# Optimization experiments

Hardware: AMD Instinct MI355X
Metric: run time of the kernel (lower is better)

Reference implementation:

```python
import jax, jax.numpy as jnp
import numpy as np

B, S, D, H = 2, 2048, 1024, 16
DH = D // H

def setup_inputs() -> dict:
    key = jax.random.key(0)
    ks = jax.random.split(key, 12)
    def lin(kw, kb, fan_in):
        bound = 1.0 / np.sqrt(fan_in)
        W = jax.random.uniform(kw, (D, D), jnp.float32, -bound, bound)
        b = jax.random.uniform(kb, (D,), jnp.float32, -bound, bound)
        return W, b
    Wq, bq = lin(ks[0], ks[1], D)
    Wk, bk = lin(ks[2], ks[3], D)
    Wv, bv = lin(ks[4], ks[5], D)
    Wo, bo = lin(ks[6], ks[7], D)
    q = jax.random.normal(ks[8], (B, S, D), jnp.float32)
    k = jax.random.normal(ks[9], (B, S, D), jnp.float32)
    v = jax.random.normal(ks[10], (B, S, D), jnp.float32)
    # causal mask (1 = keep, 0 = masked), broadcastable to [B,H,S,S]
    mask = jnp.tril(jnp.ones((S, S), jnp.int32))[None, None, :, :]
    return {"q": q, "k": k, "v": v, "mask": mask,
            "Wq": Wq, "bq": bq, "Wk": Wk, "bk": bk,
            "Wv": Wv, "bv": bv, "Wo": Wo, "bo": bo}

def reference(q, k, v, mask, Wq, bq, Wk, bk, Wv, bv, Wo, bo):
    # projections: torch Linear is x @ W.T + b
    def split(x):  # [B,S,D] -> [B,H,S,DH]
        return x.reshape(B, S, H, DH).transpose(0, 2, 1, 3)
    qh = split(q @ Wq.T + bq)
    kh = split(k @ Wk.T + bk)
    vh = split(v @ Wv.T + bv)
    score = jnp.einsum('bhqd,bhkd->bhqk', qh, kh) / jnp.sqrt(jnp.float32(DH))
    score = jnp.where(mask == 0, jnp.float32(-1e9), score)
    attn = jax.nn.softmax(score, axis=-1)
    out = jnp.einsum('bhqk,bhkd->bhqd', attn, vh)
    out = out.transpose(0, 2, 1, 3).reshape(B, S, D)
    return out @ Wo.T + bo, attn
```

## Files before the change

kernel.cpp:

```cpp
#include <hip/hip_runtime.h>

#define S_LEN 2048
#define D_MODEL 1024
#define N_HEADS 16
#define D_HEAD 64
#define BATCH 2

typedef __bf16 bf16;
typedef __bf16 bf16x8 __attribute__((ext_vector_type(8)));
typedef __bf16 bf16x4 __attribute__((ext_vector_type(4)));
typedef float f32x4 __attribute__((ext_vector_type(4)));

__device__ __forceinline__ f32x4 mfma16(bf16x8 a, bf16x8 b, f32x4 c) {
  return __builtin_amdgcn_mfma_f32_16x16x32_bf16(a, b, c, 0, 0, 0);
}

__device__ __forceinline__ void gload16(const bf16* g, bf16* lds) {
  __builtin_amdgcn_global_load_lds((const __attribute__((address_space(1))) void*)g,
                                   (__attribute__((address_space(3))) void*)lds, 16, 0, 0);
}

__global__ __launch_bounds__(256) void cvt_w(
    const float* __restrict__ s0, const float* __restrict__ s1,
    const float* __restrict__ s2, const float* __restrict__ s3,
    bf16* __restrict__ d0, bf16* __restrict__ d1, bf16* __restrict__ d2,
    bf16* __restrict__ d3) {
  const int y = blockIdx.y;
  const float* s = (y == 0) ? s0 : (y == 1) ? s1 : (y == 2) ? s2 : s3;
  bf16* d = (y == 0) ? d0 : (y == 1) ? d1 : (y == 2) ? d2 : d3;
  const int i = blockIdx.x * blockDim.x + threadIdx.x;
  const f32x4 a = *(const f32x4*)(s + (size_t)i * 8);
  const f32x4 b = *(const f32x4*)(s + (size_t)i * 8 + 4);
  bf16x8 o;
  o[0] = (bf16)a[0]; o[1] = (bf16)a[1]; o[2] = (bf16)a[2]; o[3] = (bf16)a[3];
  o[4] = (bf16)b[0]; o[5] = (bf16)b[1]; o[6] = (bf16)b[2]; o[7] = (bf16)b[3];
  *(bf16x8*)(d + (size_t)i * 8) = o;
}

__device__ __forceinline__ void gemm_loop(const bf16* __restrict__ gA,
                                          const bf16* __restrict__ gB,
                                          bf16* As, bf16* Bs,
                                          f32x4 (&acc)[4][4], int tid) {
  const int l = tid & 63;
  const int w = tid >> 6;
  const int wr = w >> 1, wc = w & 1;
  const int lr = l & 15, lg = l >> 4;
  const int rl = l >> 2;
  const int c8l = l & 3;
  const int chA = lg ^ ((lr >> 1) & 3);

#define STAGE_PAIR(ks, buf)                                                   \
  {                                                                           \
    _Pragma("unroll") for (int i = 0; i < 2; ++i) {                           \
      const int blk = w + i * 4;                                              \
      const int row = blk * 16 + rl;                                          \
      const int s8 = c8l ^ ((row >> 1) & 3);                                  \
      gload16(gA + (size_t)row * D_MODEL + (ks) * 32 + s8 * 8,                \
              As + (buf) * 4096 + blk * 512);                                 \
      gload16(gB + (size_t)row * D_MODEL + (ks) * 32 + s8 * 8,                \
              Bs + (buf) * 4096 + blk * 512);                                 \
    }                                                                         \
  }

  STAGE_PAIR(0, 0);
  __syncthreads();
  int cur = 0;
  for (int ks = 0; ks < 32; ++ks) {
    if (ks < 31) STAGE_PAIR(ks + 1, cur ^ 1);
    bf16x8 af[4], bfb[4];
#pragma unroll
    for (int mm = 0; mm < 4; ++mm)
      af[mm] = *(const bf16x8*)(As + cur * 4096 + (wr * 64 + mm * 16 + lr) * 32 + chA * 8);
#pragma unroll
    for (int nn = 0; nn < 4; ++nn)
      bfb[nn] = *(const bf16x8*)(Bs + cur * 4096 + (wc * 64 + nn * 16 + lr) * 32 + chA * 8);
#pragma unroll
    for (int mm = 0; mm < 4; ++mm)
#pragma unroll
      for (int nn = 0; nn < 4; ++nn)
        acc[mm][nn] = mfma16(af[mm], bfb[nn], acc[mm][nn]);
    __syncthreads();
    cur ^= 1;
  }
#undef STAGE_PAIR
}

__device__ __forceinline__ void gemm_loop_af32(const float* __restrict__ gA32,
                                               const bf16* __restrict__ gB,
                                               bf16* As, bf16* Bs,
                                               f32x4 (&acc)[4][4], int tid) {
  const int l = tid & 63;
  const int w = tid >> 6;
  const int wr = w >> 1, wc = w & 1;
  const int lr = l & 15, lg = l >> 4;
  const int rl = l >> 2, c8l = l & 3;
  const int chA = lg ^ ((lr >> 1) & 3);

  const int arow = tid >> 1;
  const int ahalf = tid & 1;
  const float* aptr = gA32 + (size_t)arow * D_MODEL + ahalf * 16;
  const int asw = (arow >> 1) & 3;

#define LOAD_A(ks, av)                                                        \
  _Pragma("unroll") for (int c = 0; c < 4; ++c)                               \
      av[c] = *(const f32x4*)(aptr + (ks) * 32 + c * 4);

#define WRITE_A(buf, av)                                                      \
  {                                                                           \
    _Pragma("unroll") for (int j = 0; j < 2; ++j) {                           \
      bf16x8 o;                                                               \
      _Pragma("unroll") for (int e = 0; e < 4; ++e) {                         \
        o[e] = (bf16)av[j * 2][e];                                            \
        o[e + 4] = (bf16)av[j * 2 + 1][e];                                    \
      }                                                                       \
      const int c8 = ahalf * 2 + j;                                           \
      *(bf16x8*)(As + (buf) * 4096 + arow * 32 + (c8 ^ asw) * 8) = o;         \
    }                                                                         \
  }

#define STAGE_B(ks, buf)                                                      \
  {                                                                           \
    _Pragma("unroll") for (int i = 0; i < 2; ++i) {                           \
      const int blk = w + i * 4;                                              \
      const int row = blk * 16 + rl;                                          \
      const int s8 = c8l ^ ((row >> 1) & 3);                                  \
      gload16(gB + (size_t)row * D_MODEL + (ks) * 32 + s8 * 8,                \
              Bs + (buf) * 4096 + blk * 512);                                 \
    }                                                                         \
  }

  {
    f32x4 av[4];
    LOAD_A(0, av);
    STAGE_B(0, 0);
    WRITE_A(0, av);
  }
  __syncthreads();
  int cur = 0;
  for (int ks = 0; ks < 32; ++ks) {
    f32x4 av[4];
    if (ks < 31) {
      LOAD_A(ks + 1, av);
      STAGE_B(ks + 1, cur ^ 1);
    }
    bf16x8 af[4], bfb[4];
#pragma unroll
    for (int mm = 0; mm < 4; ++mm)
      af[mm] = *(const bf16x8*)(As + cur * 4096 + (wr * 64 + mm * 16 + lr) * 32 + chA * 8);
#pragma unroll
    for (int nn = 0; nn < 4; ++nn)
      bfb[nn] = *(const bf16x8*)(Bs + cur * 4096 + (wc * 64 + nn * 16 + lr) * 32 + chA * 8);
#pragma unroll
    for (int mm = 0; mm < 4; ++mm)
#pragma unroll
      for (int nn = 0; nn < 4; ++nn)
        acc[mm][nn] = mfma16(af[mm], bfb[nn], acc[mm][nn]);
    if (ks < 31) WRITE_A(cur ^ 1, av);
    __syncthreads();
    cur ^= 1;
  }
#undef LOAD_A
#undef WRITE_A
#undef STAGE_B
}

__global__ __launch_bounds__(256) void gemm_qkv(
    const float* __restrict__ qf, const float* __restrict__ kf,
    const float* __restrict__ vf, const bf16* __restrict__ Wqb,
    const bf16* __restrict__ Wkb, const bf16* __restrict__ Wvb,
    const float* __restrict__ biasq, const float* __restrict__ biask,
    const float* __restrict__ biasv, bf16* __restrict__ qhw,
    bf16* __restrict__ khw, bf16* __restrict__ vtw) {
  __shared__ __align__(16) char smem[32768];
  bf16* As = (bf16*)smem;
  bf16* Bs = (bf16*)(smem + 16384);
  typedef bf16 Trow[72];
  Trow* T = (Trow*)smem;
  const int z = blockIdx.z;
  const float* A = (z == 0) ? qf : (z == 1) ? kf : vf;
  const bf16* W = (z == 0) ? Wqb : (z == 1) ? Wkb : Wvb;
  const float* bias = (z == 0) ? biasq : (z == 1) ? biask : biasv;
  const float scale = (z == 0) ? 0.125f : 1.0f;
  bf16* out = (z == 0) ? qhw : (z == 1) ? khw : vtw;

  const int tid = threadIdx.x;
  const int l = tid & 63;
  const int w = tid >> 6;
  const int wr = w >> 1, wc = w & 1;
  const int lr = l & 15, lg = l >> 4;

  f32x4 acc[4][4] = {};
  gemm_loop_af32(A + ((size_t)blockIdx.x * 128) * D_MODEL,
                 W + ((size_t)blockIdx.y * 128) * D_MODEL, As, Bs, acc, tid);

  const int b = (blockIdx.x * 128) >> 11;
  const int s0 = (blockIdx.x * 128) & 2047;

  if (z == 2) {
#pragma unroll
    for (int half = 0; half < 2; ++half) {
      if (wc == half) {
#pragma unroll
        for (int nn = 0; nn < 4; ++nn) {
          const int n = blockIdx.y * 128 + half * 64 + nn * 16 + lr;
          const float bv = bias[n];
#pragma unroll
          for (int mm = 0; mm < 4; ++mm)
#pragma unroll
            for (int r = 0; r < 4; ++r) {
              const int ml = wr * 64 + mm * 16 + lg * 4 + r;
              T[ml][nn * 16 + lr] = (bf16)(acc[mm][nn][r] + bv);
            }
        }
      }
      __syncthreads();
      const int d = tid & 63;
      const int sblk = (tid >> 6) * 32;
      const int hglob = blockIdx.y * 2 + half;
      bf16* orow = vtw + (((size_t)(b * N_HEADS + hglob)) * D_HEAD + d) * S_LEN + s0 + sblk;
#pragma unroll
      for (int j = 0; j < 4; ++j) {
        bf16x8 pk;
#pragma unroll
        for (int e = 0; e < 8; ++e) pk[e] = T[sblk + j * 8 + e][d];
        *(bf16x8*)(orow + j * 8) = pk;
      }
      __syncthreads();
    }
  } else {
#pragma unroll
    for (int half = 0; half < 2; ++half) {
      if (wc == half) {
#pragma unroll
        for (int nn = 0; nn < 4; ++nn) {
          const int n = blockIdx.y * 128 + half * 64 + nn * 16 + lr;
          const float bv = bias[n];
#pragma unroll
          for (int mm = 0; mm < 4; ++mm)
#pragma unroll
            for (int r = 0; r < 4; ++r) {
              const int ml = wr * 64 + mm * 16 + lg * 4 + r;
              T[ml][nn * 16 + lr] = (bf16)((acc[mm][nn][r] + bv) * scale);
            }
        }
      }
      __syncthreads();
      const int hglob = blockIdx.y * 2 + half;
      bf16* obase = out + ((size_t)(b * N_HEADS + hglob) * S_LEN + s0) * D_HEAD;
      const int rsub = tid >> 3;
      const int d8 = (tid & 7) * 8;
#pragma unroll
      for (int j = 0; j < 4; ++j) {
        const int row_l = j * 32 + rsub;
        *(bf16x8*)(obase + (size_t)row_l * D_HEAD + d8) = *(const bf16x8*)(&T[row_l][d8]);
      }
      __syncthreads();
    }
  }
}

__device__ __forceinline__ void stage_strip(const bf16* __restrict__ src,
                                            size_t rstride, bf16* lds, int tid) {
#pragma unroll
  for (int rnd = 0; rnd < 2; ++rnd) {
    const int chunk = rnd * 256 + tid;
    const int row = chunk >> 3;
    const int c8 = chunk & 7;
    const int src8 = c8 ^ (row & 7);
    gload16(src + (size_t)row * rstride + src8 * 8, lds + chunk * 8);
  }
}

__global__ __launch_bounds__(256) void attn_flash(
    const bf16* __restrict__ qh, const bf16* __restrict__ kh,
    const bf16* __restrict__ vt, bf16* __restrict__ ctx,
    float* __restrict__ lbuf, float* __restrict__ attn) {
  __shared__ bf16 Kb[2][64 * 64];
  __shared__ bf16 Vb[2][64 * 64];
  __shared__ bf16 P[4][16][72];
  const int tid = threadIdx.x;
  const int w = tid >> 6, l = tid & 63;
  const int lr = l & 15, lg = l >> 4;
  const int bh = blockIdx.y;
  const int bxx = blockIdx.x;

  if (bxx >= 32) {
    int rem = bxx - 32, zq = 0, cnt = 7;
    while (rem >= cnt) { rem -= cnt; --cnt; ++zq; }
    const int kq = zq + 1 + rem;
    float* base = attn + (size_t)bh * S_LEN * S_LEN + (size_t)(zq * 256) * S_LEN + kq * 256;
    const f32x4 zv = {};
    for (int it = 0; it < 64; ++it) {
      float* rp = base + (size_t)(it * 4 + w) * S_LEN + l * 4;
      __builtin_nontemporal_store(zv, (f32x4*)rp);
    }
    return;
  }

  const int qgroup = (bxx & 1) ? (31 - (bxx >> 1)) : (bxx >> 1);
  const int q0 = qgroup * 64 + w * 16;
  const int qrow = q0 + lr;
  const bf16* qp = qh + (size_t)bh * S_LEN * D_HEAD;
  const bf16* kp = kh + (size_t)bh * S_LEN * D_HEAD;
  const bf16* vp = vt + (size_t)bh * D_HEAD * S_LEN;

  const bf16x8 qf0 = *(const bf16x8*)(qp + (size_t)qrow * D_HEAD + lg * 8);
  const bf16x8 qf1 = *(const bf16x8*)(qp + (size_t)qrow * D_HEAD + 32 + lg * 8);

  const float NINF = -__builtin_inff();
  const int nfull = qgroup;
  const int x0 = (lg ^ (lr & 7)) * 8;
  const int x1 = ((4 | lg) ^ (lr & 7)) * 8;

  stage_strip(kp, D_HEAD, Kb[0], tid);
  stage_strip(vp, S_LEN, Vb[0], tid);
  __syncthreads();

  float lsum = 0.f;
  f32x4 oacc[4] = {};
  int cur = 0;

  for (int st = 0; st < nfull; ++st) {
    stage_strip(kp + (size_t)(st + 1) * 64 * D_HEAD, D_HEAD, Kb[cur ^ 1], tid);
    stage_strip(vp + (st + 1) * 64, S_LEN, Vb[cur ^ 1], tid);

    float ps = 0.f;
    __builtin_amdgcn_s_setprio(1);
    f32x4 zz4[4];
#pragma unroll
    for (int t = 0; t < 4; ++t) {
      const bf16* krow = Kb[cur] + (t * 16 + lr) * 64;
      f32x4 zz = {};
      zz = mfma16(*(const bf16x8*)(krow + x0), qf0, zz);
      zz = mfma16(*(const bf16x8*)(krow + x1), qf1, zz);
      zz4[t] = zz;
    }
    __builtin_amdgcn_s_setprio(0);
#pragma unroll
    for (int t = 0; t < 4; ++t) {
      bf16x4 pk;
#pragma unroll
      for (int r = 0; r < 4; ++r) {
        const float e = __expf(fminf(zz4[t][r], 60.f));
        ps += e;
        pk[r] = (bf16)e;
      }
      *(bf16x4*)(&P[w][lr][t * 16 + lg * 4]) = pk;
    }
    ps += __shfl_xor(ps, 16);
    ps += __shfl_xor(ps, 32);
    lsum += ps;
    const bf16x8 pb0 = *(const bf16x8*)(&P[w][lr][lg * 8]);
    const bf16x8 pb1 = *(const bf16x8*)(&P[w][lr][32 + lg * 8]);
    __builtin_amdgcn_s_setprio(1);
#pragma unroll
    for (int dt = 0; dt < 4; ++dt) {
      const bf16* vrow = Vb[cur] + (dt * 16 + lr) * 64;
      oacc[dt] = mfma16(*(const bf16x8*)(vrow + x0), pb0, oacc[dt]);
      oacc[dt] = mfma16(*(const bf16x8*)(vrow + x1), pb1, oacc[dt]);
    }
    __builtin_amdgcn_s_setprio(0);
    __syncthreads();
    cur ^= 1;
  }

  {
    float ps = 0.f;
#pragma unroll
    for (int t = 0; t < 4; ++t) {
      bf16x4 pk;
      if (t <= w) {
        const bf16* krow = Kb[cur] + (t * 16 + lr) * 64;
        f32x4 zz = {};
        zz = mfma16(*(const bf16x8*)(krow + x0), qf0, zz);
        zz = mfma16(*(const bf16x8*)(krow + x1), qf1, zz);
#pragma unroll
        for (int r = 0; r < 4; ++r) {
          const float sv = (t == w && (lg * 4 + r) > lr) ? NINF : zz[r];
          const float e = __expf(fminf(sv, 60.f));
          ps += e;
          pk[r] = (bf16)e;
        }
      } else {
#pragma unroll
        for (int r = 0; r < 4; ++r) pk[r] = (bf16)0.f;
      }
      *(bf16x4*)(&P[w][lr][t * 16 + lg * 4]) = pk;
    }
    ps += __shfl_xor(ps, 16);
    ps += __shfl_xor(ps, 32);
    lsum += ps;
    const bf16x8 pb0 = *(const bf16x8*)(&P[w][lr][lg * 8]);
    const bf16x8 pb1 = *(const bf16x8*)(&P[w][lr][32 + lg * 8]);
#pragma unroll
    for (int dt = 0; dt < 4; ++dt) {
      const bf16* vrow = Vb[cur] + (dt * 16 + lr) * 64;
      oacc[dt] = mfma16(*(const bf16x8*)(vrow + x0), pb0, oacc[dt]);
      oacc[dt] = mfma16(*(const bf16x8*)(vrow + x1), pb1, oacc[dt]);
    }
  }

  const float invl = 1.0f / lsum;
  const int b = bh >> 4, h = bh & 15;
  bf16* crow = ctx + ((size_t)(b * S_LEN + qrow)) * D_MODEL + h * D_HEAD;
#pragma unroll
  for (int dt = 0; dt < 4; ++dt) {
    bf16x4 ov;
#pragma unroll
    for (int r = 0; r < 4; ++r) ov[r] = (bf16)(oacc[dt][r] * invl);
    *(bf16x4*)(crow + dt * 16 + lg * 4) = ov;
  }
  if (lg == 0) lbuf[(size_t)bh * S_LEN + qrow] = invl;
}

__global__ __launch_bounds__(256) void mat_out(
    const bf16* __restrict__ qh, const bf16* __restrict__ kh,
    const float* __restrict__ lbuf, float* __restrict__ attn,
    const bf16* __restrict__ ctxA, const bf16* __restrict__ Wo,
    const float* __restrict__ bo, float* __restrict__ outp) {
  __shared__ __align__(16) char smem[34048];
  const int bid = blockIdx.x;
  const int tid = threadIdx.x;
  const int w = tid >> 6, l = tid & 63;
  const int lr = l & 15, lg = l >> 4;

  if (bid < 256) {
    bf16* As = (bf16*)smem;
    bf16* Bs = (bf16*)(smem + 16384);
    const int bx = bid & 31, by = bid >> 5;
    const int wr = w >> 1, wc = w & 1;
    f32x4 acc[4][4] = {};
    gemm_loop(ctxA + ((size_t)bx * 128) * D_MODEL,
              Wo + ((size_t)by * 128) * D_MODEL, As, Bs, acc, tid);
    const int rowg0 = bx * 128 + wr * 64;
    const int colg0 = by * 128 + wc * 64;
#pragma unroll
    for (int nn = 0; nn < 4; ++nn) {
      const int n = colg0 + nn * 16 + lr;
      const float bv = bo[n];
#pragma unroll
      for (int mm = 0; mm < 4; ++mm)
#pragma unroll
        for (int r = 0; r < 4; ++r) {
          const int m = rowg0 + mm * 16 + lg * 4 + r;
          __builtin_nontemporal_store(acc[mm][nn][r] + bv,
                                      outp + (size_t)m * D_MODEL + n);
        }
    }
    return;
  }

  bf16* Pt = (bf16*)smem;
  const int mid = bid - 256;
  const int bh = mid / 144;
  int rem = mid - bh * 144;
  int g = 0;
  while (2 * (g + 1) * (g + 2) <= rem) ++g;
  const int rem2 = rem - 2 * g * (g + 1);
  const int q0t = 4 * g + rem2 / (g + 1);
  const int kq = rem2 - (g + 1) * (rem2 / (g + 1));
  const int q0 = q0t * 64;
  const int k0b = kq * 256;
  float* ap = attn + (size_t)bh * S_LEN * S_LEN;

  const int k0 = k0b + w * 64;
  if (k0 <= q0 + 63) {
    const bf16* qp = qh + (size_t)bh * S_LEN * D_HEAD;
    const bf16* kp = kh + (size_t)bh * S_LEN * D_HEAD;
    float iv[4];
#pragma unroll
    for (int qs = 0; qs < 4; ++qs)
      iv[qs] = lbuf[(size_t)bh * S_LEN + q0 + qs * 16 + lr];
    bf16x8 kf[4][2], qf[4][2];
#pragma unroll
    for (int kt = 0; kt < 4; ++kt) {
      kf[kt][0] = *(const bf16x8*)(kp + (size_t)(k0 + kt * 16 + lr) * D_HEAD + lg * 8);
      kf[kt][1] = *(const bf16x8*)(kp + (size_t)(k0 + kt * 16 + lr) * D_HEAD + 32 + lg * 8);
    }
#pragma unroll
    for (int qs = 0; qs < 4; ++qs) {
      qf[qs][0] = *(const bf16x8*)(qp + (size_t)(q0 + qs * 16 + lr) * D_HEAD + lg * 8);
      qf[qs][1] = *(const bf16x8*)(qp + (size_t)(q0 + qs * 16 + lr) * D_HEAD + 32 + lg * 8);
    }
    f32x4 acc[4][4] = {};
#pragma unroll
    for (int qs = 0; qs < 4; ++qs)
#pragma unroll
      for (int kt = 0; kt < 4; ++kt) {
        acc[qs][kt] = mfma16(kf[kt][0], qf[qs][0], acc[qs][kt]);
        acc[qs][kt] = mfma16(kf[kt][1], qf[qs][1], acc[qs][kt]);
      }
#pragma unroll
    for (int qs = 0; qs < 4; ++qs) {
      const int q = q0 + qs * 16 + lr;
#pragma unroll
      for (int kt = 0; kt < 4; ++kt) {
        const int kbase = k0 + kt * 16 + lg * 4;
        bf16x4 pk;
#pragma unroll
        for (int r = 0; r < 4; ++r) {
          const float pv = (kbase + r > q)
                               ? 0.f
                               : __expf(fminf(acc[qs][kt][r], 60.f)) * iv[qs];
          pk[r] = (bf16)pv;
        }
        *(bf16x4*)(Pt + (qs * 16 + lr) * 264 + w * 64 + kt * 16 + lg * 4) = pk;
      }
    }
  } else {
    const bf16x4 z4 = {};
#pragma unroll
    for (int j = 0; j < 16; ++j)
      *(bf16x4*)(Pt + (j * 4 + lg) * 264 + w * 64 + lr * 4) = z4;
  }
  __syncthreads();

#pragma unroll
  for (int j = 0; j < 16; ++j) {
    const int rowl = w * 16 + j;
    const bf16x4 pk = *(const bf16x4*)(Pt + rowl * 264 + l * 4);
    f32x4 o;
    o[0] = (float)pk[0]; o[1] = (float)pk[1];
    o[2] = (float)pk[2]; o[3] = (float)pk[3];
    __builtin_nontemporal_store(
        o, (f32x4*)(ap + (size_t)(q0 + rowl) * S_LEN + k0b + l * 4));
  }
}

extern "C" void kernel_launch(void* const* d_in, const int* in_sizes, int n_in,
                              void* d_out, int out_size, void* d_ws, size_t ws_size,
                              hipStream_t stream) {
  (void)in_sizes; (void)n_in; (void)out_size; (void)ws_size;
  const float* q  = (const float*)d_in[0];
  const float* k  = (const float*)d_in[1];
  const float* v  = (const float*)d_in[2];
  const float* Wq = (const float*)d_in[4];
  const float* bq = (const float*)d_in[5];
  const float* Wk = (const float*)d_in[6];
  const float* bk = (const float*)d_in[7];
  const float* Wv = (const float*)d_in[8];
  const float* bv = (const float*)d_in[9];
  const float* Wo = (const float*)d_in[10];
  const float* bo = (const float*)d_in[11];

  float* outp = (float*)d_out;
  float* attn = outp + (size_t)BATCH * S_LEN * D_MODEL;

  char* ws = (char*)d_ws;
  bf16* qhw  = (bf16*)(ws);
  bf16* khw  = (bf16*)(ws + (8u << 20));
  bf16* vtw  = (bf16*)(ws + (16u << 20));
  bf16* ctxb = (bf16*)(ws + (24u << 20));
  bf16* Wqb  = (bf16*)(ws + (32u << 20));
  bf16* Wkb  = (bf16*)(ws + (34u << 20));
  bf16* Wvb  = (bf16*)(ws + (36u << 20));
  bf16* Wob  = (bf16*)(ws + (38u << 20));
  float* lbuf = (float*)(ws + (40u << 20));

  dim3 bb(256);
  cvt_w<<<dim3(512, 4), bb, 0, stream>>>(Wq, Wk, Wv, Wo, Wqb, Wkb, Wvb, Wob);
  gemm_qkv<<<dim3(32, 8, 3), bb, 0, stream>>>(q, k, v, Wqb, Wkb, Wvb,
                                              bq, bk, bv, qhw, khw, vtw);
  attn_flash<<<dim3(60, 32), bb, 0, stream>>>(qhw, khw, vtw, ctxb, lbuf, attn);
  mat_out<<<dim3(256 + 4608), bb, 0, stream>>>(qhw, khw, lbuf, attn,
                                               ctxb, Wob, bo, outp);
}
```

Measured before the change: 236.6 us.

## Fuse attention-probability writeback into flash kernel via second K pass

The flash attention kernel now does a second pass over K after computing the row normalizer. It recomputes QK^T, normalizes the scores and writes the probability matrix (plus zeros for the masked tail) directly, instead of leaving that to a separate kernel that read lbuf. This removes the lbuf buffer and the extra launch that mixed the output GEMM with attention-map tiles, and the output GEMM becomes a standalone launch. The cost is that flash blocks now recompute QK and carry the large fp32 attention store serially, which could lengthen the critical path and worsen load imbalance across blocks.

Measured after the change: 241.3 us. No clear change (+2.0%).

```diff
diff --git a/kernel.cpp b/kernel.cpp
--- a/kernel.cpp
+++ b/kernel.cpp
@@ -271,10 +271,10 @@
   }
 }
 
-__global__ __launch_bounds__(256) void attn_flash(
+__global__ __launch_bounds__(256) void attn_fused(
     const bf16* __restrict__ qh, const bf16* __restrict__ kh,
     const bf16* __restrict__ vt, bf16* __restrict__ ctx,
-    float* __restrict__ lbuf, float* __restrict__ attn) {
+    float* __restrict__ attn) {
   __shared__ bf16 Kb[2][64 * 64];
   __shared__ bf16 Vb[2][64 * 64];
   __shared__ bf16 P[4][16][72];
@@ -303,12 +303,14 @@
   const bf16* qp = qh + (size_t)bh * S_LEN * D_HEAD;
   const bf16* kp = kh + (size_t)bh * S_LEN * D_HEAD;
   const bf16* vp = vt + (size_t)bh * D_HEAD * S_LEN;
+  float* ap = attn + (size_t)bh * S_LEN * S_LEN;
 
   const bf16x8 qf0 = *(const bf16x8*)(qp + (size_t)qrow * D_HEAD + lg * 8);
   const bf16x8 qf1 = *(const bf16x8*)(qp + (size_t)qrow * D_HEAD + 32 + lg * 8);
 
   const float NINF = -__builtin_inff();
   const int nfull = qgroup;
+  const int ktail = ((qgroup >> 2) << 2) + 4;
   const int x0 = (lg ^ (lr & 7)) * 8;
   const int x1 = ((4 | lg) ^ (lr & 7)) * 8;
 
@@ -410,120 +412,121 @@
     for (int r = 0; r < 4; ++r) ov[r] = (bf16)(oacc[dt][r] * invl);
     *(bf16x4*)(crow + dt * 16 + lg * 4) = ov;
   }
-  if (lg == 0) lbuf[(size_t)bh * S_LEN + qrow] = invl;
-}
-
-__global__ __launch_bounds__(256) void mat_out(
-    const bf16* __restrict__ qh, const bf16* __restrict__ kh,
-    const float* __restrict__ lbuf, float* __restrict__ attn,
-    const bf16* __restrict__ ctxA, const bf16* __restrict__ Wo,
-    const float* __restrict__ bo, float* __restrict__ outp) {
-  __shared__ __align__(16) char smem[34048];
-  const int bid = blockIdx.x;
+
+  stage_strip(kp, D_HEAD, Kb[cur ^ 1], tid);
+  __syncthreads();
+  cur ^= 1;
+
+  for (int st = 0; st < nfull; ++st) {
+    stage_strip(kp + (size_t)(st + 1) * 64 * D_HEAD, D_HEAD, Kb[cur ^ 1], tid);
+    __builtin_amdgcn_s_setprio(1);
+    f32x4 zz4[4];
+#pragma unroll
+    for (int t = 0; t < 4; ++t) {
+      const bf16* krow = Kb[cur] + (t * 16 + lr) * 64;
+      f32x4 zz = {};
+      zz = mfma16(*(const bf16x8*)(krow + x0), qf0, zz);
+      zz = mfma16(*(const bf16x8*)(krow + x1), qf1, zz);
+      zz4[t] = zz;
+    }
+    __builtin_amdgcn_s_setprio(0);
+#pragma unroll
+    for (int t = 0; t < 4; ++t) {
+      bf16x4 pk;
+#pragma unroll
+      for (int r = 0; r < 4; ++r)
+        pk[r] = (bf16)(__expf(fminf(zz4[t][r], 60.f)) * invl);
+      *(bf16x4*)(&P[w][lr][t * 16 + lg * 4]) = pk;
+    }
+#pragma unroll
+    for (int j = 0; j < 4; ++j) {
+      const int row = j * 4 + lg;
+      const bf16x4 pk4 = *(const bf16x4*)(&P[w][row][lr * 4]);
+      f32x4 o;
+      o[0] = (float)pk4[0]; o[1] = (float)pk4[1];
+      o[2] = (float)pk4[2]; o[3] = (float)pk4[3];
+      __builtin_nontemporal_store(
+          o, (f32x4*)(ap + (size_t)(q0 + row) * S_LEN + st * 64 + lr * 4));
+    }
+    __syncthreads();
+    cur ^= 1;
+  }
+
+  {
+    const int st = nfull;
+#pragma unroll
+    for (int t = 0; t < 4; ++t) {
+      bf16x4 pk;
+      if (t <= w) {
+        const bf16* krow = Kb[cur] + (t * 16 + lr) * 64;
+        f32x4 zz = {};
+        zz = mfma16(*(const bf16x8*)(krow + x0), qf0, zz);
+        zz = mfma16(*(const bf16x8*)(krow + x1), qf1, zz);
+#pragma unroll
+        for (int r = 0; r < 4; ++r) {
+          const float sv = (t == w && (lg * 4 + r) > lr) ? NINF : zz[r];
+          pk[r] = (bf16)(__expf(fminf(sv, 60.f)) * invl);
+        }
+      } else {
+#pragma unroll
+        for (int r = 0; r < 4; ++r) pk[r] = (bf16)0.f;
+      }
+      *(bf16x4*)(&P[w][lr][t * 16 + lg * 4]) = pk;
+    }
+#pragma unroll
+    for (int j = 0; j < 4; ++j) {
+      const int row = j * 4 + lg;
+      const bf16x4 pk4 = *(const bf16x4*)(&P[w][row][lr * 4]);
+      f32x4 o;
+      o[0] = (float)pk4[0]; o[1] = (float)pk4[1];
+      o[2] = (float)pk4[2]; o[3] = (float)pk4[3];
+      __builtin_nontemporal_store(
+          o, (f32x4*)(ap + (size_t)(q0 + row) * S_LEN + st * 64 + lr * 4));
+    }
+  }
+
+  for (int st = nfull + 1; st < ktail; ++st) {
+    const f32x4 zv = {};
+#pragma unroll
+    for (int j = 0; j < 4; ++j) {
+      const int row = j * 4 + lg;
+      __builtin_nontemporal_store(
+          zv, (f32x4*)(ap + (size_t)(q0 + row) * S_LEN + st * 64 + lr * 4));
+    }
+  }
+}
+
+__global__ __launch_bounds__(256) void gemm_out(const bf16* __restrict__ A,
+                                                const bf16* __restrict__ W,
+                                                const float* __restrict__ bias,
+                                                float* __restrict__ out) {
+  __shared__ __align__(16) char smem[32768];
+  bf16* As = (bf16*)smem;
+  bf16* Bs = (bf16*)(smem + 16384);
   const int tid = threadIdx.x;
-  const int w = tid >> 6, l = tid & 63;
+  const int l = tid & 63;
+  const int w = tid >> 6;
+  const int wr = w >> 1, wc = w & 1;
   const int lr = l & 15, lg = l >> 4;
 
-  if (bid < 256) {
-    bf16* As = (bf16*)smem;
-    bf16* Bs = (bf16*)(smem + 16384);
-    const int bx = bid & 31, by = bid >> 5;
-    const int wr = w >> 1, wc = w & 1;
-    f32x4 acc[4][4] = {};
-    gemm_loop(ctxA + ((size_t)bx * 128) * D_MODEL,
-              Wo + ((size_t)by * 128) * D_MODEL, As, Bs, acc, tid);
-    const int rowg0 = bx * 128 + wr * 64;
-    const int colg0 = by * 128 + wc * 64;
-#pragma unroll
-    for (int nn = 0; nn < 4; ++nn) {
-      const int n = colg0 + nn * 16 + lr;
-      const float bv = bo[n];
-#pragma unroll
-      for (int mm = 0; mm < 4; ++mm)
-#pragma unroll
-        for (int r = 0; r < 4; ++r) {
-          const int m = rowg0 + mm * 16 + lg * 4 + r;
-          __builtin_nontemporal_store(acc[mm][nn][r] + bv,
-                                      outp + (size_t)m * D_MODEL + n);
-        }
-    }
-    return;
-  }
-
-  bf16* Pt = (bf16*)smem;
-  const int mid = bid - 256;
-  const int bh = mid / 144;
-  int rem = mid - bh * 144;
-  int g = 0;
-  while (2 * (g + 1) * (g + 2) <= rem) ++g;
-  const int rem2 = rem - 2 * g * (g + 1);
-  const int q0t = 4 * g + rem2 / (g + 1);
-  const int kq = rem2 - (g + 1) * (rem2 / (g + 1));
-  const int q0 = q0t * 64;
-  const int k0b = kq * 256;
-  float* ap = attn + (size_t)bh * S_LEN * S_LEN;
-
-  const int k0 = k0b + w * 64;
-  if (k0 <= q0 + 63) {
-    const bf16* qp = qh + (size_t)bh * S_LEN * D_HEAD;
-    const bf16* kp = kh + (size_t)bh * S_LEN * D_HEAD;
-    float iv[4];
-#pragma unroll
-    for (int qs = 0; qs < 4; ++qs)
-      iv[qs] = lbuf[(size_t)bh * S_LEN + q0 + qs * 16 + lr];
-    bf16x8 kf[4][2], qf[4][2];
-#pragma unroll
-    for (int kt = 0; kt < 4; ++kt) {
-      kf[kt][0] = *(const bf16x8*)(kp + (size_t)(k0 + kt * 16 + lr) * D_HEAD + lg * 8);
-      kf[kt][1] = *(const bf16x8*)(kp + (size_t)(k0 + kt * 16 + lr) * D_HEAD + 32 + lg * 8);
-    }
-#pragma unroll
-    for (int qs = 0; qs < 4; ++qs) {
-      qf[qs][0] = *(const bf16x8*)(qp + (size_t)(q0 + qs * 16 + lr) * D_HEAD + lg * 8);
-      qf[qs][1] = *(const bf16x8*)(qp + (size_t)(q0 + qs * 16 + lr) * D_HEAD + 32 + lg * 8);
-    }
-    f32x4 acc[4][4] = {};
-#pragma unroll
-    for (int qs = 0; qs < 4; ++qs)
-#pragma unroll
-      for (int kt = 0; kt < 4; ++kt) {
-        acc[qs][kt] = mfma16(kf[kt][0], qf[qs][0], acc[qs][kt]);
-        acc[qs][kt] = mfma16(kf[kt][1], qf[qs][1], acc[qs][kt]);
-      }
-#pragma unroll
-    for (int qs = 0; qs < 4; ++qs) {
-      const int q = q0 + qs * 16 + lr;
-#pragma unroll
-      for (int kt = 0; kt < 4; ++kt) {
-        const int kbase = k0 + kt * 16 + lg * 4;
-        bf16x4 pk;
-#pragma unroll
-        for (int r = 0; r < 4; ++r) {
-          const float pv = (kbase + r > q)
-                               ? 0.f
-                               : __expf(fminf(acc[qs][kt][r], 60.f)) * iv[qs];
-          pk[r] = (bf16)pv;
-        }
-        *(bf16x4*)(Pt + (qs * 16 + lr) * 264 + w * 64 + kt * 16 + lg * 4) = pk;
-      }
-    }
-  } else {
-    const bf16x4 z4 = {};
-#pragma unroll
-    for (int j = 0; j < 16; ++j)
-      *(bf16x4*)(Pt + (j * 4 + lg) * 264 + w * 64 + lr * 4) = z4;
-  }
-  __syncthreads();
-
-#pragma unroll
-  for (int j = 0; j < 16; ++j) {
-    const int rowl = w * 16 + j;
-    const bf16x4 pk = *(const bf16x4*)(Pt + rowl * 264 + l * 4);
-    f32x4 o;
-    o[0] = (float)pk[0]; o[1] = (float)pk[1];
-    o[2] = (float)pk[2]; o[3] = (float)pk[3];
-    __builtin_nontemporal_store(
-        o, (f32x4*)(ap + (size_t)(q0 + rowl) * S_LEN + k0b + l * 4));
+  f32x4 acc[4][4] = {};
+  gemm_loop(A + ((size_t)blockIdx.x * 128) * D_MODEL,
+            W + ((size_t)blockIdx.y * 128) * D_MODEL, As, Bs, acc, tid);
+
+  const int rowg0 = blockIdx.x * 128 + wr * 64;
+  const int colg0 = blockIdx.y * 128 + wc * 64;
+#pragma unroll
+  for (int nn = 0; nn < 4; ++nn) {
+    const int n = colg0 + nn * 16 + lr;
+    const float bv = bias[n];
+#pragma unroll
+    for (int mm = 0; mm < 4; ++mm)
+#pragma unroll
+      for (int r = 0; r < 4; ++r) {
+        const int m = rowg0 + mm * 16 + lg * 4 + r;
+        __builtin_nontemporal_store(acc[mm][nn][r] + bv,
+                                    out + (size_t)m * D_MODEL + n);
+      }
   }
 }
 
@@ -555,13 +558,11 @@
   bf16* Wkb  = (bf16*)(ws + (34u << 20));
   bf16* Wvb  = (bf16*)(ws + (36u << 20));
   bf16* Wob  = (bf16*)(ws + (38u << 20));
-  float* lbuf = (float*)(ws + (40u << 20));
 
   dim3 bb(256);
   cvt_w<<<dim3(512, 4), bb, 0, stream>>>(Wq, Wk, Wv, Wo, Wqb, Wkb, Wvb, Wob);
   gemm_qkv<<<dim3(32, 8, 3), bb, 0, stream>>>(q, k, v, Wqb, Wkb, Wvb,
                                               bq, bk, bv, qhw, khw, vtw);
-  attn_flash<<<dim3(60, 32), bb, 0, stream>>>(qhw, khw, vtw, ctxb, lbuf, attn);
-  mat_out<<<dim3(256 + 4608), bb, 0, stream>>>(qhw, khw, lbuf, attn,
-                                               ctxb, Wob, bo, outp);
-}
+  attn_fused<<<dim3(60, 32), bb, 0, stream>>>(qhw, khw, vtw, ctxb, attn);
+  gemm_out<<<dim3(32, 8), bb, 0, stream>>>(ctxb, Wob, bo, outp);
+}
```
